# Kernel tuning notes

Hardware: AMD Instinct MI355X
Metric: run time of the kernel (lower is better)

## Reference

```python
import jax, jax.numpy as jnp
import numpy as np

T, B, IN, H, OUT = 128, 1024, 47, 646, 5

def setup_inputs() -> dict:
    key = jax.random.key(0)
    ks = jax.random.split(key, 11)
    s_in = 1.0 / np.sqrt(H)
    return {
        "xs": jax.random.normal(ks[0], (T, B, IN), dtype=jnp.float32),
        "W_ih0": jax.random.normal(ks[1], (H, IN), dtype=jnp.float32) * s_in,
        "W_hh0": jax.random.normal(ks[2], (H, H), dtype=jnp.float32) * s_in,
        "b_ih0": jax.random.normal(ks[3], (H,), dtype=jnp.float32) * s_in,
        "b_hh0": jax.random.normal(ks[4], (H,), dtype=jnp.float32) * s_in,
        "W_ih1": jax.random.normal(ks[5], (H, H), dtype=jnp.float32) * s_in,
        "W_hh1": jax.random.normal(ks[6], (H, H), dtype=jnp.float32) * s_in,
        "b_ih1": jax.random.normal(ks[7], (H,), dtype=jnp.float32) * s_in,
        "b_hh1": jax.random.normal(ks[8], (H,), dtype=jnp.float32) * s_in,
        "W_out": jax.random.normal(ks[9], (OUT, H), dtype=jnp.float32) * s_in,
        "b_out": jnp.zeros((OUT,), dtype=jnp.float32),
    }

def reference(xs, W_ih0, W_hh0, b_ih0, b_hh0, W_ih1, W_hh1, b_ih1, b_hh1, W_out, b_out):
    batch = xs.shape[1]
    h0 = jnp.zeros((batch, H), dtype=xs.dtype)
    h1 = jnp.zeros((batch, H), dtype=xs.dtype)

    def step(carry, x_t):
        h0, h1 = carry
        # layer 0: Elman cell, tanh
        h0 = jnp.tanh(x_t @ W_ih0.T + b_ih0 + h0 @ W_hh0.T + b_hh0)
        # layer 1 consumes layer 0's output at this timestep
        h1 = jnp.tanh(h0 @ W_ih1.T + b_ih1 + h1 @ W_hh1.T + b_hh1)
        return (h0, h1), None

    (h0, h1), _ = jax.lax.scan(step, (h0, h1), xs)
    # classifier on last layer's final hidden state
    logits = h1 @ W_out.T + b_out  # [B, 5]
    return logits
```

## Files before the change

### kernel.cpp

```cpp
#include <hip/hip_runtime.h>
#include <hip/hip_bf16.h>

#define T_STEPS 128
#define B_SZ    1024
#define IN_SZ   47
#define H_SZ    646
#define OUT_SZ  5

#define XK    96
#define K0    768
#define K1    1344
#define N0PAD 704
#define N1PAD 672
#define RING  17
#define SLAB  172032
#define PH    129

typedef __hip_bfloat16 bf16;
typedef unsigned short ush;
using frag8 = __attribute__((ext_vector_type(8))) short;
using f32x4 = __attribute__((ext_vector_type(4))) float;


__global__ void prep_xs(const float* __restrict__ xs, bf16* __restrict__ xs_pad) {
    int idx = blockIdx.x * blockDim.x + threadIdx.x;
    if (idx >= T_STEPS * B_SZ * XK) return;
    int k = idx % XK;
    int rb = idx / XK;
    float v = (k < IN_SZ) ? xs[(size_t)rb * IN_SZ + k] : 0.f;
    xs_pad[idx] = __float2bfloat16(v);
}

__global__ void pack_w0(const float* __restrict__ Wih, const float* __restrict__ Whh,
                        bf16* __restrict__ Wc) {
    int idx = blockIdx.x * blockDim.x + threadIdx.x;
    if (idx >= N0PAD * K0) return;
    int j = idx / K0, k = idx % K0;
    float v = 0.f;
    if (j < H_SZ) {
        if (k < IN_SZ)                      v = Wih[(size_t)j * IN_SZ + k];
        else if (k >= XK && k < XK + H_SZ)  v = Whh[(size_t)j * H_SZ + (k - XK)];
    }
    Wc[idx] = __float2bfloat16(v);
}

__global__ void pack_w1(const float* __restrict__ Wih, const float* __restrict__ Whh,
                        bf16* __restrict__ Wc) {
    int idx = blockIdx.x * blockDim.x + threadIdx.x;
    if (idx >= N1PAD * K1) return;
    int j = idx / K1, k = idx % K1;
    float v = 0.f;
    if (j < H_SZ) {
        if (k < H_SZ)                          v = Wih[(size_t)j * H_SZ + k];
        else if (k >= 672 && k < 672 + H_SZ)   v = Whh[(size_t)j * H_SZ + (k - 672)];
    }
    Wc[idx] = __float2bfloat16(v);
}

__global__ void pack_bias(const float* __restrict__ bi, const float* __restrict__ bh,
                          float* __restrict__ b, int n) {
    int j = blockIdx.x * blockDim.x + threadIdx.x;
    if (j >= n) return;
    b[j] = (j < H_SZ) ? (bi[j] + bh[j]) : 0.f;
}


__device__ __forceinline__ void tanh_store(ush* dst, float x) {
    x = fminf(fmaxf(x, -15.f), 15.f);
    float e = __expf(2.f * x);
    bf16 hb = __float2bfloat16((e - 1.f) / (e + 1.f));
    __hip_atomic_store(dst, *(ush*)&hb, __ATOMIC_RELAXED, __HIP_MEMORY_SCOPE_AGENT);
}

__global__ __launch_bounds__(256, 1) void persist(
    const bf16* __restrict__ xs_pad, const bf16* __restrict__ Wc0,
    const bf16* __restrict__ Wc1, const float* __restrict__ b0,
    const float* __restrict__ b1, bf16* __restrict__ Sring,
    int* __restrict__ flags)
{
    extern __shared__ ush Wlds[];
    const int bid  = blockIdx.x;
    const int rg   = bid & 7;
    const int c8   = bid >> 3;
    const bool isL0 = (c8 < 11);
    const int wave = threadIdx.x >> 6;
    const int lane = threadIdx.x & 63;
    const int q8   = (lane >> 4) * 8;
    const int l15  = lane & 15;

    if (isL0) {
        const int col0 = c8 * 64;
        for (int g = wave; g < 96; g += 4) {
            int kc = g >> 2, ct = g & 3;
            const bf16* src = Wc0 + (size_t)(col0 + ct*16 + l15) * K0 + kc*32 + q8;
            *(uint4*)&Wlds[g*512 + lane*8] = *(const uint4*)src;
        }
    } else {
        const int col0 = (c8 - 11) * 32;
        for (int g = wave; g < 84; g += 4) {
            int kc = g >> 1, ct = g & 1;
            const bf16* src = Wc1 + (size_t)(col0 + ct*16 + l15) * K1 + kc*32 + q8;
            *(uint4*)&Wlds[g*512 + lane*8] = *(const uint4*)src;
        }
    }
    __syncthreads();

    float bias[4];
    int col0;
    if (isL0) {
        col0 = c8 * 64;
        #pragma unroll
        for (int ct = 0; ct < 4; ++ct) bias[ct] = b0[col0 + ct*16 + l15];
    } else {
        col0 = (c8 - 11) * 32;
        #pragma unroll
        for (int ct = 0; ct < 2; ++ct) bias[ct] = b1[col0 + ct*16 + l15];
    }
    const int loc0 = wave * 32 + l15;
    const int loc1 = loc0 + 16;
    bf16* const ringbase = Sring + (size_t)rg * RING * SLAB;
    int*  const flagbase = flags + rg * PH;

    for (int p = 0; p <= 128; ++p) {
        if (p > 0) {
            if (threadIdx.x == 0) {
                while (__hip_atomic_load(&flagbase[p-1], __ATOMIC_RELAXED,
                                         __HIP_MEMORY_SCOPE_AGENT) < 32)
                    __builtin_amdgcn_s_sleep(2);
            }
            __syncthreads();
            if (p >= RING + 1 && (p - 1) % RING == 0)
                __builtin_amdgcn_fence(__ATOMIC_ACQUIRE, "agent");
        }
        const bf16* rsl = ringbase + (size_t)((p + RING - 1) % RING) * SLAB;
        bf16*       wsl = ringbase + (size_t)(p % RING) * SLAB;
        const bool active = isL0 ? (p < 128) : (p >= 1);

        if (active) {
            if (isL0) {
                const bf16* xsb = xs_pad + ((size_t)p * B_SZ + rg*128) * XK;
                const bf16* x0  = xsb + (size_t)loc0 * XK + q8;
                const bf16* x1  = xsb + (size_t)loc1 * XK + q8;
                const bf16* h0p = rsl + (size_t)loc0 * K1 + q8;
                const bf16* h1p = rsl + (size_t)loc1 * K1 + q8;
                f32x4 acc[2][4] = {};
                auto ldA = [&](int kc, int r) -> uint4 {
                    if (kc < 3) return *(const uint4*)((r ? x1 : x0) + kc*32);
                    return *(const uint4*)((r ? h1p : h0p) + (kc-3)*32);
                };
                uint4 ac[2], an[2];
                ac[0] = ldA(0,0); ac[1] = ldA(0,1);
                an[0] = ldA(1,0); an[1] = ldA(1,1);
                #pragma unroll
                for (int kc = 0; kc < 24; ++kc) {
                    uint4 a2[2];
                    if (kc + 2 < 24) { a2[0] = ldA(kc+2,0); a2[1] = ldA(kc+2,1); }
                    else             { a2[0] = ac[0];       a2[1] = ac[1]; }
                    #pragma unroll
                    for (int ct = 0; ct < 4; ++ct) {
                        frag8 wf = *(const frag8*)&Wlds[(kc*4+ct)*512 + lane*8];
                        acc[0][ct] = __builtin_amdgcn_mfma_f32_16x16x32_bf16(
                            *(const frag8*)&ac[0], wf, acc[0][ct], 0,0,0);
                        acc[1][ct] = __builtin_amdgcn_mfma_f32_16x16x32_bf16(
                            *(const frag8*)&ac[1], wf, acc[1][ct], 0,0,0);
                    }
                    ac[0]=an[0]; ac[1]=an[1]; an[0]=a2[0]; an[1]=a2[1];
                }
                #pragma unroll
                for (int r = 0; r < 2; ++r) {
                    const int rbase = wave*32 + r*16 + (lane>>4)*4;
                    #pragma unroll
                    for (int ct = 0; ct < 4; ++ct) {
                        const int col = col0 + ct*16 + l15;
                        if (col < H_SZ) {
                            #pragma unroll
                            for (int i = 0; i < 4; ++i)
                                tanh_store((ush*)(wsl + (size_t)(rbase+i)*K1 + col),
                                           acc[r][ct][i] + bias[ct]);
                        }
                    }
                }
            } else {
                const bf16* a0 = rsl + (size_t)loc0 * K1 + q8;
                const bf16* a1 = rsl + (size_t)loc1 * K1 + q8;
                f32x4 acc[2][2] = {};
                uint4 ac[2], an[2];
                ac[0] = *(const uint4*)(a0);      ac[1] = *(const uint4*)(a1);
                an[0] = *(const uint4*)(a0 + 32); an[1] = *(const uint4*)(a1 + 32);
                #pragma unroll
                for (int kc = 0; kc < 42; ++kc) {
                    uint4 a2[2];
                    if (kc + 2 < 42) { a2[0] = *(const uint4*)(a0 + (kc+2)*32);
                                       a2[1] = *(const uint4*)(a1 + (kc+2)*32); }
                    else             { a2[0] = ac[0]; a2[1] = ac[1]; }
                    #pragma unroll
                    for (int ct = 0; ct < 2; ++ct) {
                        frag8 wf = *(const frag8*)&Wlds[(kc*2+ct)*512 + lane*8];
                        acc[0][ct] = __builtin_amdgcn_mfma_f32_16x16x32_bf16(
                            *(const frag8*)&ac[0], wf, acc[0][ct], 0,0,0);
                        acc[1][ct] = __builtin_amdgcn_mfma_f32_16x16x32_bf16(
                            *(const frag8*)&ac[1], wf, acc[1][ct], 0,0,0);
                    }
                    ac[0]=an[0]; ac[1]=an[1]; an[0]=a2[0]; an[1]=a2[1];
                }
                #pragma unroll
                for (int r = 0; r < 2; ++r) {
                    const int rbase = wave*32 + r*16 + (lane>>4)*4;
                    #pragma unroll
                    for (int ct = 0; ct < 2; ++ct) {
                        const int col = col0 + ct*16 + l15;
                        if (col < H_SZ) {
                            #pragma unroll
                            for (int i = 0; i < 4; ++i)
                                tanh_store((ush*)(wsl + (size_t)(rbase+i)*K1 + 672 + col),
                                           acc[r][ct][i] + bias[ct]);
                        }
                    }
                }
            }
        }
        __syncthreads();
        if (threadIdx.x == 0)
            __hip_atomic_fetch_add(&flagbase[p], 1, __ATOMIC_RELAXED,
                                   __HIP_MEMORY_SCOPE_AGENT);
    }
}

__global__ __launch_bounds__(256) void classifier(
    const bf16* __restrict__ Sring, const float* __restrict__ Wout,
    const float* __restrict__ bout, float* __restrict__ out)
{
    const int wave = threadIdx.x >> 6, lane = threadIdx.x & 63;
    const int row = blockIdx.x * 4 + wave;
    const int rg = row >> 7, loc = row & 127;
    const bf16* h1 = Sring + ((size_t)rg * RING + (128 % RING)) * SLAB
                     + (size_t)loc * K1 + 672;
    float acc[OUT_SZ] = {0.f, 0.f, 0.f, 0.f, 0.f};
    for (int k = lane; k < H_SZ; k += 64) {
        float h = __bfloat162float(h1[k]);
        #pragma unroll
        for (int o = 0; o < OUT_SZ; ++o) acc[o] += h * Wout[(size_t)o * H_SZ + k];
    }
    #pragma unroll
    for (int o = 0; o < OUT_SZ; ++o) {
        float v = acc[o];
        #pragma unroll
        for (int off = 32; off; off >>= 1) v += __shfl_down(v, off, 64);
        if (lane == 0) out[(size_t)row * OUT_SZ + o] = v + bout[o];
    }
}


extern "C" void kernel_launch(void* const* d_in, const int* in_sizes, int n_in,
                              void* d_out, int out_size, void* d_ws, size_t ws_size,
                              hipStream_t stream) {
    const float* xs   = (const float*)d_in[0];
    const float* Wih0 = (const float*)d_in[1];
    const float* Whh0 = (const float*)d_in[2];
    const float* bih0 = (const float*)d_in[3];
    const float* bhh0 = (const float*)d_in[4];
    const float* Wih1 = (const float*)d_in[5];
    const float* Whh1 = (const float*)d_in[6];
    const float* bih1 = (const float*)d_in[7];
    const float* bhh1 = (const float*)d_in[8];
    const float* Wout = (const float*)d_in[9];
    const float* bout = (const float*)d_in[10];
    float* out = (float*)d_out;

    char* ws = (char*)d_ws;
    size_t off = 0;
    bf16* xs_pad = (bf16*)(ws + off); off += (size_t)T_STEPS * B_SZ * XK * 2;
    bf16* Wc0    = (bf16*)(ws + off); off += (size_t)N0PAD * K0 * 2;
    bf16* Wc1    = (bf16*)(ws + off); off += (size_t)N1PAD * K1 * 2;
    float* b0    = (float*)(ws + off); off += (size_t)N0PAD * 4;
    float* b1    = (float*)(ws + off); off += (size_t)N1PAD * 4;
    bf16* Sring  = (bf16*)(ws + off); off += (size_t)8 * RING * SLAB * 2;
    int*  flags  = (int*)(ws + off);  off += (size_t)8 * PH * 4;

    hipMemsetAsync(Sring, 0, (size_t)8 * RING * SLAB * 2, stream);
    hipMemsetAsync(flags, 0, (size_t)8 * PH * 4, stream);

    prep_xs <<<(T_STEPS * B_SZ * XK + 255) / 256, 256, 0, stream>>>(xs, xs_pad);
    pack_w0 <<<(N0PAD * K0 + 255) / 256, 256, 0, stream>>>(Wih0, Whh0, Wc0);
    pack_w1 <<<(N1PAD * K1 + 255) / 256, 256, 0, stream>>>(Wih1, Whh1, Wc1);
    pack_bias<<<(N0PAD + 255) / 256, 256, 0, stream>>>(bih0, bhh0, b0, N0PAD);
    pack_bias<<<(N1PAD + 255) / 256, 256, 0, stream>>>(bih1, bhh1, b1, N1PAD);

    hipFuncSetAttribute((const void*)persist,
                        hipFuncAttributeMaxDynamicSharedMemorySize, 98304);
    void* args[] = { (void*)&xs_pad, (void*)&Wc0, (void*)&Wc1, (void*)&b0,
                     (void*)&b1, (void*)&Sring, (void*)&flags };
    hipLaunchCooperativeKernel((const void*)persist, dim3(256), dim3(256),
                               args, 98304, stream);

    classifier<<<B_SZ / 4, 256, 0, stream>>>(Sring, Wout, bout, out);
}
```

Baseline: 1.976 ms.

## Use 8 waves per block with one 16-row tile each and deeper A prefetch

The persistent kernel now launches 512 threads per block instead of 256, so each of the 8 waves owns 16 batch rows instead of 32. The per-wave MFMA loop carries half as many accumulators. The A-operand prefetch ring grows to 4 stages, so global/L2 reads of the recurrent state run further ahead of the MFMAs. This raises per-step latency hiding and wave-level parallelism, but each LDS weight fragment is now reused across only one row tile per wave, doubling LDS weight reads, and the larger block may add register pressure.

New measurement: 1.711 ms. 1.15x faster.

```diff
diff --git a/kernel.cpp b/kernel.cpp
--- a/kernel.cpp
+++ b/kernel.cpp
@@ -72,7 +72,7 @@
     __hip_atomic_store(dst, *(ush*)&hb, __ATOMIC_RELAXED, __HIP_MEMORY_SCOPE_AGENT);
 }
 
-__global__ __launch_bounds__(256, 1) void persist(
+__global__ __launch_bounds__(512, 2) void persist(
     const bf16* __restrict__ xs_pad, const bf16* __restrict__ Wc0,
     const bf16* __restrict__ Wc1, const float* __restrict__ b0,
     const float* __restrict__ b1, bf16* __restrict__ Sring,
@@ -83,21 +83,21 @@
     const int rg   = bid & 7;
     const int c8   = bid >> 3;
     const bool isL0 = (c8 < 11);
-    const int wave = threadIdx.x >> 6;
+    const int wv   = threadIdx.x >> 6;
     const int lane = threadIdx.x & 63;
     const int q8   = (lane >> 4) * 8;
     const int l15  = lane & 15;
 
     if (isL0) {
         const int col0 = c8 * 64;
-        for (int g = wave; g < 96; g += 4) {
+        for (int g = wv; g < 96; g += 8) {
             int kc = g >> 2, ct = g & 3;
             const bf16* src = Wc0 + (size_t)(col0 + ct*16 + l15) * K0 + kc*32 + q8;
             *(uint4*)&Wlds[g*512 + lane*8] = *(const uint4*)src;
         }
     } else {
         const int col0 = (c8 - 11) * 32;
-        for (int g = wave; g < 84; g += 4) {
+        for (int g = wv; g < 84; g += 8) {
             int kc = g >> 1, ct = g & 1;
             const bf16* src = Wc1 + (size_t)(col0 + ct*16 + l15) * K1 + kc*32 + q8;
             *(uint4*)&Wlds[g*512 + lane*8] = *(const uint4*)src;
@@ -116,8 +116,7 @@
         #pragma unroll
         for (int ct = 0; ct < 2; ++ct) bias[ct] = b1[col0 + ct*16 + l15];
     }
-    const int loc0 = wave * 32 + l15;
-    const int loc1 = loc0 + 16;
+    const int loc = wv * 16 + l15;
     bf16* const ringbase = Sring + (size_t)rg * RING * SLAB;
     int*  const flagbase = flags + rg * PH;
 
@@ -138,83 +137,69 @@
 
         if (active) {
             if (isL0) {
-                const bf16* xsb = xs_pad + ((size_t)p * B_SZ + rg*128) * XK;
-                const bf16* x0  = xsb + (size_t)loc0 * XK + q8;
-                const bf16* x1  = xsb + (size_t)loc1 * XK + q8;
-                const bf16* h0p = rsl + (size_t)loc0 * K1 + q8;
-                const bf16* h1p = rsl + (size_t)loc1 * K1 + q8;
-                f32x4 acc[2][4] = {};
-                auto ldA = [&](int kc, int r) -> uint4 {
-                    if (kc < 3) return *(const uint4*)((r ? x1 : x0) + kc*32);
-                    return *(const uint4*)((r ? h1p : h0p) + (kc-3)*32);
-                };
-                uint4 ac[2], an[2];
-                ac[0] = ldA(0,0); ac[1] = ldA(0,1);
-                an[0] = ldA(1,0); an[1] = ldA(1,1);
+                const bf16* xr = xs_pad + ((size_t)p * B_SZ + rg*128 + loc) * XK + q8;
+                const bf16* hr = rsl + (size_t)loc * K1 + q8;
+                f32x4 acc[4] = {};
+                uint4 abuf[4];
+                #pragma unroll
+                for (int i = 0; i < 4; ++i)
+                    abuf[i] = (i < 3) ? *(const uint4*)(xr + i*32)
+                                      : *(const uint4*)(hr + (i-3)*32);
                 #pragma unroll
                 for (int kc = 0; kc < 24; ++kc) {
-                    uint4 a2[2];
-                    if (kc + 2 < 24) { a2[0] = ldA(kc+2,0); a2[1] = ldA(kc+2,1); }
-                    else             { a2[0] = ac[0];       a2[1] = ac[1]; }
+                    uint4 acur = abuf[kc & 3];
+                    if (kc + 4 < 24) {
+                        int kn = kc + 4;
+                        abuf[kc & 3] = (kn < 3) ? *(const uint4*)(xr + kn*32)
+                                                : *(const uint4*)(hr + (kn-3)*32);
+                    }
+                    frag8 af = *(const frag8*)&acur;
                     #pragma unroll
                     for (int ct = 0; ct < 4; ++ct) {
                         frag8 wf = *(const frag8*)&Wlds[(kc*4+ct)*512 + lane*8];
-                        acc[0][ct] = __builtin_amdgcn_mfma_f32_16x16x32_bf16(
-                            *(const frag8*)&ac[0], wf, acc[0][ct], 0,0,0);
-                        acc[1][ct] = __builtin_amdgcn_mfma_f32_16x16x32_bf16(
-                            *(const frag8*)&ac[1], wf, acc[1][ct], 0,0,0);
-                    }
-                    ac[0]=an[0]; ac[1]=an[1]; an[0]=a2[0]; an[1]=a2[1];
-                }
-                #pragma unroll
-                for (int r = 0; r < 2; ++r) {
-                    const int rbase = wave*32 + r*16 + (lane>>4)*4;
-                    #pragma unroll
-                    for (int ct = 0; ct < 4; ++ct) {
-                        const int col = col0 + ct*16 + l15;
-                        if (col < H_SZ) {
-                            #pragma unroll
-                            for (int i = 0; i < 4; ++i)
-                                tanh_store((ush*)(wsl + (size_t)(rbase+i)*K1 + col),
-                                           acc[r][ct][i] + bias[ct]);
-                        }
+                        acc[ct] = __builtin_amdgcn_mfma_f32_16x16x32_bf16(
+                            af, wf, acc[ct], 0, 0, 0);
+                    }
+                }
+                const int rbase = wv*16 + (lane>>4)*4;
+                #pragma unroll
+                for (int ct = 0; ct < 4; ++ct) {
+                    const int col = col0 + ct*16 + l15;
+                    if (col < H_SZ) {
+                        #pragma unroll
+                        for (int i = 0; i < 4; ++i)
+                            tanh_store((ush*)(wsl + (size_t)(rbase+i)*K1 + col),
+                                       acc[ct][i] + bias[ct]);
                     }
                 }
             } else {
-                const bf16* a0 = rsl + (size_t)loc0 * K1 + q8;
-                const bf16* a1 = rsl + (size_t)loc1 * K1 + q8;
-                f32x4 acc[2][2] = {};
-                uint4 ac[2], an[2];
-                ac[0] = *(const uint4*)(a0);      ac[1] = *(const uint4*)(a1);
-                an[0] = *(const uint4*)(a0 + 32); an[1] = *(const uint4*)(a1 + 32);
+                const bf16* ar = rsl + (size_t)loc * K1 + q8;
+                f32x4 acc[2] = {};
+                uint4 abuf[4];
+                #pragma unroll
+                for (int i = 0; i < 4; ++i) abuf[i] = *(const uint4*)(ar + i*32);
                 #pragma unroll
                 for (int kc = 0; kc < 42; ++kc) {
-                    uint4 a2[2];
-                    if (kc + 2 < 42) { a2[0] = *(const uint4*)(a0 + (kc+2)*32);
-                                       a2[1] = *(const uint4*)(a1 + (kc+2)*32); }
-                    else             { a2[0] = ac[0]; a2[1] = ac[1]; }
+                    uint4 acur = abuf[kc & 3];
+                    if (kc + 4 < 42)
+                        abuf[kc & 3] = *(const uint4*)(ar + (kc+4)*32);
+                    frag8 af = *(const frag8*)&acur;
                     #pragma unroll
                     for (int ct = 0; ct < 2; ++ct) {
                         frag8 wf = *(const frag8*)&Wlds[(kc*2+ct)*512 + lane*8];
-                        acc[0][ct] = __builtin_amdgcn_mfma_f32_16x16x32_bf16(
-                            *(const frag8*)&ac[0], wf, acc[0][ct], 0,0,0);
-                        acc[1][ct] = __builtin_amdgcn_mfma_f32_16x16x32_bf16(
-                            *(const frag8*)&ac[1], wf, acc[1][ct], 0,0,0);
-                    }
-                    ac[0]=an[0]; ac[1]=an[1]; an[0]=a2[0]; an[1]=a2[1];
-                }
-                #pragma unroll
-                for (int r = 0; r < 2; ++r) {
-                    const int rbase = wave*32 + r*16 + (lane>>4)*4;
-                    #pragma unroll
-                    for (int ct = 0; ct < 2; ++ct) {
-                        const int col = col0 + ct*16 + l15;
-                        if (col < H_SZ) {
-                            #pragma unroll
-                            for (int i = 0; i < 4; ++i)
-                                tanh_store((ush*)(wsl + (size_t)(rbase+i)*K1 + 672 + col),
-                                           acc[r][ct][i] + bias[ct]);
-                        }
+                        acc[ct] = __builtin_amdgcn_mfma_f32_16x16x32_bf16(
+                            af, wf, acc[ct], 0, 0, 0);
+                    }
+                }
+                const int rbase = wv*16 + (lane>>4)*4;
+                #pragma unroll
+                for (int ct = 0; ct < 2; ++ct) {
+                    const int col = col0 + ct*16 + l15;
+                    if (col < H_SZ) {
+                        #pragma unroll
+                        for (int i = 0; i < 4; ++i)
+                            tanh_store((ush*)(wsl + (size_t)(rbase+i)*K1 + 672 + col),
+                                       acc[ct][i] + bias[ct]);
                     }
                 }
             }
@@ -290,7 +275,7 @@
                         hipFuncAttributeMaxDynamicSharedMemorySize, 98304);
     void* args[] = { (void*)&xs_pad, (void*)&Wc0, (void*)&Wc1, (void*)&b0,
                      (void*)&b1, (void*)&Sring, (void*)&flags };
-    hipLaunchCooperativeKernel((const void*)persist, dim3(256), dim3(256),
+    hipLaunchCooperativeKernel((const void*)persist, dim3(256), dim3(512),
                                args, 98304, stream);
 
     classifier<<<B_SZ / 4, 256, 0, stream>>>(Sring, Wout, bout, out);
```
